# Optimization experiments

Measured on AMD Instinct MI355X. Metric: run time of the kernel, lower is better.

## Reference

```python
import jax, jax.numpy as jnp
import numpy as np

B, IN, OUT = 2048, 64, 2048


def setup_inputs() -> dict:
    key = jax.random.key(0)
    k1, k2, k3 = jax.random.split(key, 3)
    x = jax.random.normal(k1, (B, IN), dtype=jnp.float32)
    # learned params (shapes per init: means [in, out], inv_std_dev [out, in, in])
    means = jax.random.uniform(k2, (IN, OUT), dtype=jnp.float32)
    # roughly like the inverse of a diagonal step matrix plus small noise
    inv_std_dev = (jax.random.normal(k3, (OUT, IN, IN), dtype=jnp.float32) * 0.05
                   + jnp.eye(IN, dtype=jnp.float32) * 0.5)
    return {"x": x, "means": means, "inv_std_dev": inv_std_dev}


def reference(x, means, inv_std_dev):
    # diff[b, o, i] = x[b, i] - means[i, o]   -> [B, OUT, IN]
    d = x[:, None, :] - means.T[None, :, :]
    # torch uses inv_std_dev.pow(2) (elementwise square), not a matrix square
    A = inv_std_dev * inv_std_dev  # [OUT, IN, IN]
    # per-neuron quadratic form: q[b, o] = d[b,o,:] @ A[o] @ d[b,o,:]
    q = jnp.einsum('boi,oij,boj->bo', d, A, d)
    return jnp.exp(-0.5 * q)  # [B, OUT]
```

## Files before the change

### kernel.cpp

```cpp
#include <hip/hip_runtime.h>
#include <hip/hip_bf16.h>

typedef __bf16 bf16x8 __attribute__((ext_vector_type(8)));
typedef float f32x16 __attribute__((ext_vector_type(16)));

#define B_N 2048
#define O_N 2048
#define K_TRI 2080
#define K_TOT 2304
#define K_STEPS 36

__device__ __forceinline__ void gld16(const void* g, void* l) {
    __builtin_amdgcn_global_load_lds(
        (const __attribute__((address_space(1))) void*)g,
        (__attribute__((address_space(3))) void*)l,
        16, 0, 0);
}

__global__ __launch_bounds__(256) void rbf_prep2(
    const float* __restrict__ inv, const float* __restrict__ means,
    const float* __restrict__ x, __bf16* __restrict__ S, __bf16* __restrict__ P)
{
    __shared__ float s[64 * 65];
    __shared__ float mld[64];
    __shared__ float uw[128];
    __shared__ unsigned short ptab[K_TRI];

    const int t = threadIdx.x;
    {
        int base = 0;
#pragma unroll 1
        for (int i = 0; i < 64; ++i) {
            if (t < 64 - i) ptab[base + t] = (unsigned short)((i << 8) | (i + t));
            base += 64 - i;
        }
    }

    if ((int)blockIdx.x < O_N) {
        const int o = blockIdx.x;
        const float4* src = (const float4*)(inv + (size_t)o * 4096);
#pragma unroll
        for (int k = 0; k < 4; ++k) {
            const int idx = k * 256 + t;
            const float4 v = src[idx];
            const int i = idx >> 4;
            const int j0 = (idx & 15) * 4;
            s[i * 65 + j0 + 0] = v.x * v.x;
            s[i * 65 + j0 + 1] = v.y * v.y;
            s[i * 65 + j0 + 2] = v.z * v.z;
            s[i * 65 + j0 + 3] = v.w * v.w;
        }
        if (t < 64) mld[t] = means[(size_t)t * O_N + o];
        __syncthreads();
        if (t < 64) {
            float u = 0.f;
#pragma unroll
            for (int i = 0; i < 64; ++i) u = fmaf(s[i * 65 + t], mld[i], u);
            uw[t] = u;
        } else if (t < 128) {
            const int j = t - 64;
            float w = 0.f;
#pragma unroll
            for (int i = 0; i < 64; ++i) w = fmaf(s[j * 65 + i], mld[i], w);
            uw[64 + j] = w;
        }
        __syncthreads();
        __bf16* Srow = S + (size_t)o * K_TOT;
#pragma unroll 1
        for (int p = t; p < K_TRI; p += 256) {
            const int ij = ptab[p];
            const int i = ij >> 8, j = ij & 255;
            const float v = (i == j) ? s[i * 65 + i]
                                     : (s[i * 65 + j] + s[j * 65 + i]);
            Srow[p] = (__bf16)v;
        }
        if (t < 64) {
            const float c = -(uw[t] + uw[64 + t]);
            const __bf16 hi = (__bf16)c;
            const __bf16 lo = (__bf16)(c - (float)hi);
            Srow[K_TRI + t] = hi;
            Srow[K_TRI + 64 + t] = hi;
            Srow[K_TRI + 128 + t] = lo;
        }
        if (t == 0) {
            float kk = 0.f;
#pragma unroll
            for (int j = 0; j < 64; ++j) kk = fmaf(uw[j], mld[j], kk);
            const __bf16 khi = (__bf16)kk;
            const __bf16 klo = (__bf16)(kk - (float)khi);
            Srow[2272] = khi;
            Srow[2273] = klo;
        }
        if (t < K_TOT - 2274) Srow[2274 + t] = (__bf16)0.f;
    } else {
        const int b = (int)blockIdx.x - O_N;
        if (t < 64) mld[t] = x[(size_t)b * 64 + t];
        __syncthreads();
        __bf16* Prow = P + (size_t)b * K_TOT;
#pragma unroll 1
        for (int p = t; p < K_TRI; p += 256) {
            const int ij = ptab[p];
            Prow[p] = (__bf16)(mld[ij >> 8] * mld[ij & 255]);
        }
        if (t < 64) {
            const float v = mld[t];
            const __bf16 hi = (__bf16)v;
            Prow[K_TRI + t] = hi;
            Prow[K_TRI + 64 + t] = (__bf16)(v - (float)hi);
            Prow[K_TRI + 128 + t] = hi;
        }
        if (t == 0) {
            Prow[2272] = (__bf16)1.f;
            Prow[2273] = (__bf16)1.f;
        }
        if (t < K_TOT - 2274) Prow[2274 + t] = (__bf16)0.f;
    }
}

__global__ __launch_bounds__(256, 4) void rbf_gemm(
    const __bf16* __restrict__ P, const __bf16* __restrict__ S,
    float* __restrict__ out)
{
    __shared__ __align__(16) char sP[2][8192];
    __shared__ __align__(16) char sS[2][8192];

    const int tid = threadIdx.x;
    const int lane = tid & 63;
    const int w = tid >> 6;
    const int wr = w >> 1, wc = w & 1;
    const int cl = lane & 31;
    const int h = lane >> 5;

    const int wg = (int)blockIdx.x;
    const int xcd = wg & 7;
    const int loc = wg >> 3;
    const int ogl = loc & 3;
    const int bg = loc >> 2;
    const int oBase = (xcd * 4 + ogl) * 64;
    const int bBase = bg * 64;

    const int L0 = tid * 16, L1 = 4096 + tid * 16;
    const int r0 = L0 >> 7, r1 = L1 >> 7;
    const int c0 = (L0 & 127) ^ ((r0 & 7) << 4);
    const int c1 = (L1 & 127) ^ ((r1 & 7) << 4);
    const char* gP0 = (const char*)P + (size_t)(bBase + r0) * (K_TOT * 2) + c0;
    const char* gP1 = (const char*)P + (size_t)(bBase + r1) * (K_TOT * 2) + c1;
    const char* gS0 = (const char*)S + (size_t)(oBase + r0) * (K_TOT * 2) + c0;
    const char* gS1 = (const char*)S + (size_t)(oBase + r1) * (K_TOT * 2) + c1;

    const int arow = wr * 32 + cl;
    const int brow = wc * 32 + cl;
    const char* aPb = &sP[0][0] + arow * 128;
    const char* aSb = &sS[0][0] + brow * 128;
    const int mA = (arow & 7) << 4;
    const int mB = (brow & 7) << 4;

    gld16(gP0, &sP[0][0] + L0);
    gld16(gP1, &sP[0][0] + L1);
    gld16(gS0, &sS[0][0] + L0);
    gld16(gS1, &sS[0][0] + L1);

    const f32x16 zz = {0.f,0.f,0.f,0.f,0.f,0.f,0.f,0.f,
                       0.f,0.f,0.f,0.f,0.f,0.f,0.f,0.f};
    f32x16 acc0 = zz, acc1 = zz;

#pragma unroll 2
    for (int st = 0; st < K_STEPS; ++st) {
        __syncthreads();
        if (st < K_STEPS - 1) {
            const int nb = (st + 1) & 1;
            const size_t go = (size_t)(st + 1) * 128;
            gld16(gP0 + go, &sP[nb][0] + L0);
            gld16(gP1 + go, &sP[nb][0] + L1);
            gld16(gS0 + go, &sS[nb][0] + L0);
            gld16(gS1 + go, &sS[nb][0] + L1);
        }
        const int bo = (st & 1) * 8192;
        const bf16x8 a0 = *(const bf16x8*)(aPb + bo + ((0  + h * 16) ^ mA));
        const bf16x8 b0 = *(const bf16x8*)(aSb + bo + ((0  + h * 16) ^ mB));
        const bf16x8 a1 = *(const bf16x8*)(aPb + bo + ((32 + h * 16) ^ mA));
        const bf16x8 b1 = *(const bf16x8*)(aSb + bo + ((32 + h * 16) ^ mB));
        const bf16x8 a2 = *(const bf16x8*)(aPb + bo + ((64 + h * 16) ^ mA));
        const bf16x8 b2 = *(const bf16x8*)(aSb + bo + ((64 + h * 16) ^ mB));
        const bf16x8 a3 = *(const bf16x8*)(aPb + bo + ((96 + h * 16) ^ mA));
        const bf16x8 b3 = *(const bf16x8*)(aSb + bo + ((96 + h * 16) ^ mB));
        __builtin_amdgcn_s_setprio(1);
        acc0 = __builtin_amdgcn_mfma_f32_32x32x16_bf16(a0, b0, acc0, 0, 0, 0);
        acc1 = __builtin_amdgcn_mfma_f32_32x32x16_bf16(a1, b1, acc1, 0, 0, 0);
        acc0 = __builtin_amdgcn_mfma_f32_32x32x16_bf16(a2, b2, acc0, 0, 0, 0);
        acc1 = __builtin_amdgcn_mfma_f32_32x32x16_bf16(a3, b3, acc1, 0, 0, 0);
        __builtin_amdgcn_s_setprio(0);
    }

    const f32x16 accv = acc0 + acc1;
#pragma unroll
    for (int r = 0; r < 16; ++r) {
        const int row = (r & 3) + 8 * (r >> 2) + 4 * h;
        out[(size_t)(bBase + wr * 32 + row) * O_N + oBase + wc * 32 + cl] =
            exp2f(accv[r] * -0.72134752044448170368f);
    }
}

extern "C" void kernel_launch(void* const* d_in, const int* in_sizes, int n_in,
                              void* d_out, int out_size, void* d_ws, size_t ws_size,
                              hipStream_t stream)
{
    const float* x = (const float*)d_in[0];
    const float* means = (const float*)d_in[1];
    const float* inv = (const float*)d_in[2];
    float* out = (float*)d_out;

    __bf16* S = (__bf16*)d_ws;
    __bf16* P = (__bf16*)((char*)d_ws + (size_t)O_N * K_TOT * sizeof(__bf16));

    rbf_prep2<<<dim3(2 * O_N), dim3(256), 0, stream>>>(inv, means, x, S, P);
    rbf_gemm<<<dim3(1024), dim3(256), 0, stream>>>(P, S, out);

    (void)in_sizes; (void)n_in; (void)out_size; (void)ws_size;
}
```

Baseline: 60.79 us.

## Enlarge GEMM tile to 128x128 with 4-stage async LDS pipeline

Each GEMM block now computes a 128x128 output tile instead of 64x64, and each wave holds a 2x2 grid of 32x32 MFMA accumulators, so every LDS fragment feeds two MFMAs. Global-to-LDS loads go through a 4-buffer ring that is two stages deep, with explicit vmcnt waits in place of the per-step __syncthreads. The LDS layout drops the XOR swizzle for a k-slice-major arrangement. In exchange the grid shrinks to 256 blocks, with only one 128 KB LDS block per CU, which lowers occupancy and may leave CUs idle.

```diff
diff --git a/kernel.cpp b/kernel.cpp
--- a/kernel.cpp
+++ b/kernel.cpp
@@ -9,6 +9,7 @@
 #define K_TRI 2080
 #define K_TOT 2304
 #define K_STEPS 36
+#define ROWB (K_TOT * 2)
 
 __device__ __forceinline__ void gld16(const void* g, void* l) {
     __builtin_amdgcn_global_load_lds(
@@ -117,12 +118,11 @@
     }
 }
 
-__global__ __launch_bounds__(256, 4) void rbf_gemm(
+__global__ __launch_bounds__(256, 1) void rbf_gemm(
     const __bf16* __restrict__ P, const __bf16* __restrict__ S,
     float* __restrict__ out)
 {
-    __shared__ __align__(16) char sP[2][8192];
-    __shared__ __align__(16) char sS[2][8192];
+    __shared__ __align__(16) char sAB[4][32768];
 
     const int tid = threadIdx.x;
     const int lane = tid & 63;
@@ -134,70 +134,82 @@
     const int wg = (int)blockIdx.x;
     const int xcd = wg & 7;
     const int loc = wg >> 3;
-    const int ogl = loc & 3;
-    const int bg = loc >> 2;
-    const int oBase = (xcd * 4 + ogl) * 64;
-    const int bBase = bg * 64;
-
-    const int L0 = tid * 16, L1 = 4096 + tid * 16;
-    const int r0 = L0 >> 7, r1 = L1 >> 7;
-    const int c0 = (L0 & 127) ^ ((r0 & 7) << 4);
-    const int c1 = (L1 & 127) ^ ((r1 & 7) << 4);
-    const char* gP0 = (const char*)P + (size_t)(bBase + r0) * (K_TOT * 2) + c0;
-    const char* gP1 = (const char*)P + (size_t)(bBase + r1) * (K_TOT * 2) + c1;
-    const char* gS0 = (const char*)S + (size_t)(oBase + r0) * (K_TOT * 2) + c0;
-    const char* gS1 = (const char*)S + (size_t)(oBase + r1) * (K_TOT * 2) + c1;
-
-    const int arow = wr * 32 + cl;
-    const int brow = wc * 32 + cl;
-    const char* aPb = &sP[0][0] + arow * 128;
-    const char* aSb = &sS[0][0] + brow * 128;
-    const int mA = (arow & 7) << 4;
-    const int mB = (brow & 7) << 4;
-
-    gld16(gP0, &sP[0][0] + L0);
-    gld16(gP1, &sP[0][0] + L1);
-    gld16(gS0, &sS[0][0] + L0);
-    gld16(gS1, &sS[0][0] + L1);
+    const int oBase = (xcd * 2 + (loc & 1)) * 128;
+    const int bBase = (loc >> 1) * 128;
+
+    const char* gsrc[8];
+    int ldst[8];
+#pragma unroll
+    for (int r = 0; r < 8; ++r) {
+        const int Ld = r * 4096 + tid * 16;
+        ldst[r] = Ld;
+        const int Lo = Ld & 16383;
+        const int ks = Lo >> 11;
+        const int row = (Lo >> 4) & 127;
+        gsrc[r] = ((Ld >> 14) ? (const char*)S + (size_t)(oBase + row) * ROWB
+                              : (const char*)P + (size_t)(bBase + row) * ROWB)
+                  + ks * 16;
+    }
+
+#define RBF_STAGE(ST) do {                                                    \
+    const size_t go_ = (size_t)(ST) * 128;                                    \
+    char* d_ = &sAB[(ST) & 3][0];                                             \
+    _Pragma("unroll")                                                         \
+    for (int r_ = 0; r_ < 8; ++r_)                                            \
+        gld16(gsrc[r_] + go_, d_ + ldst[r_]);                                 \
+} while (0)
+
+    RBF_STAGE(0);
+    RBF_STAGE(1);
 
     const f32x16 zz = {0.f,0.f,0.f,0.f,0.f,0.f,0.f,0.f,
                        0.f,0.f,0.f,0.f,0.f,0.f,0.f,0.f};
-    f32x16 acc0 = zz, acc1 = zz;
-
-#pragma unroll 2
+    f32x16 acc00 = zz, acc01 = zz, acc10 = zz, acc11 = zz;
+
+    const int aoff = (wr * 64 + cl) * 16;
+    const int boff = 16384 + (wc * 64 + cl) * 16;
+
+#pragma unroll 1
     for (int st = 0; st < K_STEPS; ++st) {
-        __syncthreads();
-        if (st < K_STEPS - 1) {
-            const int nb = (st + 1) & 1;
-            const size_t go = (size_t)(st + 1) * 128;
-            gld16(gP0 + go, &sP[nb][0] + L0);
-            gld16(gP1 + go, &sP[nb][0] + L1);
-            gld16(gS0 + go, &sS[nb][0] + L0);
-            gld16(gS1 + go, &sS[nb][0] + L1);
-        }
-        const int bo = (st & 1) * 8192;
-        const bf16x8 a0 = *(const bf16x8*)(aPb + bo + ((0  + h * 16) ^ mA));
-        const bf16x8 b0 = *(const bf16x8*)(aSb + bo + ((0  + h * 16) ^ mB));
-        const bf16x8 a1 = *(const bf16x8*)(aPb + bo + ((32 + h * 16) ^ mA));
-        const bf16x8 b1 = *(const bf16x8*)(aSb + bo + ((32 + h * 16) ^ mB));
-        const bf16x8 a2 = *(const bf16x8*)(aPb + bo + ((64 + h * 16) ^ mA));
-        const bf16x8 b2 = *(const bf16x8*)(aSb + bo + ((64 + h * 16) ^ mB));
-        const bf16x8 a3 = *(const bf16x8*)(aPb + bo + ((96 + h * 16) ^ mA));
-        const bf16x8 b3 = *(const bf16x8*)(aSb + bo + ((96 + h * 16) ^ mB));
+        if (st + 2 < K_STEPS) {
+            RBF_STAGE(st + 2);
+            asm volatile("s_waitcnt vmcnt(16)" ::: "memory");
+        } else if (st + 1 < K_STEPS) {
+            asm volatile("s_waitcnt vmcnt(8)" ::: "memory");
+        } else {
+            asm volatile("s_waitcnt vmcnt(0)" ::: "memory");
+        }
+        __builtin_amdgcn_s_barrier();
+        const char* bp = &sAB[st & 3][0];
+
         __builtin_amdgcn_s_setprio(1);
-        acc0 = __builtin_amdgcn_mfma_f32_32x32x16_bf16(a0, b0, acc0, 0, 0, 0);
-        acc1 = __builtin_amdgcn_mfma_f32_32x32x16_bf16(a1, b1, acc1, 0, 0, 0);
-        acc0 = __builtin_amdgcn_mfma_f32_32x32x16_bf16(a2, b2, acc0, 0, 0, 0);
-        acc1 = __builtin_amdgcn_mfma_f32_32x32x16_bf16(a3, b3, acc1, 0, 0, 0);
+#pragma unroll
+        for (int sl = 0; sl < 4; ++sl) {
+            const int kso = (sl * 2 + h) * 2048;
+            const bf16x8 a0 = *(const bf16x8*)(bp + kso + aoff);
+            const bf16x8 a1 = *(const bf16x8*)(bp + kso + aoff + 512);
+            const bf16x8 b0 = *(const bf16x8*)(bp + kso + boff);
+            const bf16x8 b1 = *(const bf16x8*)(bp + kso + boff + 512);
+            acc00 = __builtin_amdgcn_mfma_f32_32x32x16_bf16(a0, b0, acc00, 0, 0, 0);
+            acc01 = __builtin_amdgcn_mfma_f32_32x32x16_bf16(a0, b1, acc01, 0, 0, 0);
+            acc10 = __builtin_amdgcn_mfma_f32_32x32x16_bf16(a1, b0, acc10, 0, 0, 0);
+            acc11 = __builtin_amdgcn_mfma_f32_32x32x16_bf16(a1, b1, acc11, 0, 0, 0);
+        }
         __builtin_amdgcn_s_setprio(0);
     }
-
-    const f32x16 accv = acc0 + acc1;
+#undef RBF_STAGE
+
 #pragma unroll
     for (int r = 0; r < 16; ++r) {
-        const int row = (r & 3) + 8 * (r >> 2) + 4 * h;
-        out[(size_t)(bBase + wr * 32 + row) * O_N + oBase + wc * 32 + cl] =
-            exp2f(accv[r] * -0.72134752044448170368f);
+        const int row32 = (r & 3) + 8 * (r >> 2) + 4 * h;
+        const size_t r0 = (size_t)(bBase + wr * 64 + row32) * O_N;
+        const size_t r1 = (size_t)(bBase + wr * 64 + 32 + row32) * O_N;
+        const int c0 = oBase + wc * 64 + cl;
+        const int c1 = oBase + wc * 64 + 32 + cl;
+        out[r0 + c0] = exp2f(acc00[r] * -0.72134752044448170368f);
+        out[r0 + c1] = exp2f(acc01[r] * -0.72134752044448170368f);
+        out[r1 + c0] = exp2f(acc10[r] * -0.72134752044448170368f);
+        out[r1 + c1] = exp2f(acc11[r] * -0.72134752044448170368f);
     }
 }
 
@@ -214,7 +226,7 @@
     __bf16* P = (__bf16*)((char*)d_ws + (size_t)O_N * K_TOT * sizeof(__bf16));
 
     rbf_prep2<<<dim3(2 * O_N), dim3(256), 0, stream>>>(inv, means, x, S, P);
-    rbf_gemm<<<dim3(1024), dim3(256), 0, stream>>>(P, S, out);
+    rbf_gemm<<<dim3(256), dim3(256), 0, stream>>>(P, S, out);
 
     (void)in_sizes; (void)n_in; (void)out_size; (void)ws_size;
 }
```

Measured after the change: 69.09 us. 13.7% more time.
